# Optimization experiments

Hardware: AMD Instinct MI355X
Metric: run time of the kernel (lower is better)

Reference implementation:

```python
import jax, jax.numpy as jnp
import numpy as np

N, E, F_IN, HID, L, G, FFN = 100000, 1600000, 64, 128, 4, 512, 300
BN_EPS = 1e-5


def setup_inputs() -> dict:
    key = jax.random.key(0)
    ks = jax.random.split(key, 16)
    s = 0.05
    inp = {}
    inp["x"] = jax.random.normal(ks[0], (N, F_IN), dtype=jnp.float32)
    inp["edge_index"] = jax.random.randint(ks[1], (2, E), 0, N)
    inp["batch"] = jnp.sort(jax.random.randint(ks[2], (N,), 0, G))
    inp["enc_W"] = jax.random.normal(ks[3], (F_IN, HID), dtype=jnp.float32) * s
    inp["enc_b"] = jnp.zeros((HID,), jnp.float32)
    inp["Ws"] = jax.random.normal(ks[4], (L, HID, HID), dtype=jnp.float32) * s
    inp["bs"] = jnp.zeros((L, HID), jnp.float32)
    inp["bn_gamma"] = jnp.ones((L, HID), jnp.float32)
    inp["bn_beta"] = jnp.zeros((L, HID), jnp.float32)
    inp["bn_mean"] = jax.random.normal(ks[5], (L, HID), dtype=jnp.float32) * 0.01
    inp["bn_var"] = jnp.ones((L, HID), jnp.float32)
    inp["mlp_W0"] = jax.random.normal(ks[6], (HID, FFN), dtype=jnp.float32) * s
    inp["mlp_b0"] = jnp.zeros((FFN,), jnp.float32)
    inp["mlp_W1"] = jax.random.normal(ks[7], (FFN, FFN), dtype=jnp.float32) * s
    inp["mlp_b1"] = jnp.zeros((FFN,), jnp.float32)
    inp["mlp_W2"] = jax.random.normal(ks[8], (FFN, 1), dtype=jnp.float32) * s
    inp["mlp_b2"] = jnp.zeros((1,), jnp.float32)
    return inp


def reference(x, edge_index, batch, enc_W, enc_b, Ws, bs, bn_gamma, bn_beta,
              bn_mean, bn_var, mlp_W0, mlp_b0, mlp_W1, mlp_b1, mlp_W2, mlp_b2):
    # --- GCN normalization with self-loops (constant wrt params) ---
    loop = jnp.arange(N)
    row = jnp.concatenate([edge_index[0], loop])  # source
    col = jnp.concatenate([edge_index[1], loop])  # target (aggregation)
    deg = jax.ops.segment_sum(jnp.ones((E + N,), jnp.float32), col, num_segments=N)
    dinv = jnp.where(deg > 0, jax.lax.rsqrt(deg), 0.0)
    norm = dinv[row] * dinv[col]  # [E+N]

    # node encoder
    h = x @ enc_W + enc_b  # [N, HID]

    for i in range(L):
        h_prev = h
        # GCNConv: D^-1/2 (A+I) D^-1/2 (h W) + b
        hw = h @ Ws[i]
        msg = norm[:, None] * hw[row]                      # [E+N, HID]
        h = jax.ops.segment_sum(msg, col, num_segments=N) + bs[i]
        # BatchNorm1d (eval mode, running stats)
        h = (h - bn_mean[i]) * jax.lax.rsqrt(bn_var[i] + BN_EPS) * bn_gamma[i] + bn_beta[i]
        h = jax.nn.relu(h)
        if i > 0:
            h = h + h_prev

    # global mean pool over graphs
    sums = jax.ops.segment_sum(h, batch, num_segments=G)   # [G, HID]
    cnts = jax.ops.segment_sum(jnp.ones((N,), jnp.float32), batch, num_segments=G)
    gfeat = sums / jnp.maximum(cnts, 1.0)[:, None]

    # output MLP
    o = jax.nn.relu(gfeat @ mlp_W0 + mlp_b0)
    o = jax.nn.relu(o @ mlp_W1 + mlp_b1)
    return o @ mlp_W2 + mlp_b2  # [G, 1]
```

## Files before the change

### kernel.cpp

```cpp
#include <hip/hip_runtime.h>
#include <hip/hip_fp16.h>

#define NN 100000
#define NE 1600000
#define FIN 64
#define HID 128
#define NL 4
#define NG 512
#define FFN 300
#define BN_EPS 1e-5f
#define LDH 136
#define NB 512
#define NPB 196
#define CURPAD 16

static inline size_t alignup(size_t x) { return (x + 255) & ~(size_t)255; }

struct half8 { __half2 h[4]; };

typedef _Float16 f16;
typedef __attribute__((ext_vector_type(8))) _Float16 f16x8;
typedef __attribute__((ext_vector_type(4))) float f32x4;

__global__ __launch_bounds__(1024) void k_bcount(const int* __restrict__ col,
                                                 int* __restrict__ bcnt) {
    __shared__ int h[NB];
    int t = threadIdx.x;
    if (t < NB) h[t] = 0;
    __syncthreads();
    for (int e = blockIdx.x * 1024 + t; e < NE; e += 256 * 1024)
        atomicAdd(&h[col[e] / NPB], 1);
    __syncthreads();
    if (t < NB && h[t] > 0) atomicAdd(&bcnt[t], h[t]);
}

__global__ void k_bscan(const int* __restrict__ bcnt, int* __restrict__ bbase,
                        int* __restrict__ bcur) {
    __shared__ int s[NB];
    int t = threadIdx.x;
    int v = bcnt[t];
    s[t] = v;
    __syncthreads();
    for (int off = 1; off < NB; off <<= 1) {
        int u = (t >= off) ? s[t - off] : 0;
        __syncthreads();
        s[t] += u;
        __syncthreads();
    }
    int excl = s[t] - v;
    bbase[t] = excl;
    bcur[t * CURPAD] = excl;
    if (t == NB - 1) bbase[NB] = s[t];
}

__global__ void k_bscatter(const int* __restrict__ row, const int* __restrict__ col,
                           int* __restrict__ bcur, int* __restrict__ ebuf) {
    int e = blockIdx.x * 256 + threadIdx.x;
    if (e >= NE) return;
    int c = col[e];
    int b = c / NPB;
    int pos = atomicAdd(&bcur[b * CURPAD], 1);
    ebuf[pos] = row[e] | ((c - b * NPB) << 17);
}

__global__ __launch_bounds__(256) void k_binfill(const int* __restrict__ ebuf,
                                                 const int* __restrict__ bbase,
                                                 int* __restrict__ offs,
                                                 int* __restrict__ ends,
                                                 float* __restrict__ dinv,
                                                 int* __restrict__ csr_src) {
    __shared__ int cnt[NPB];
    __shared__ int scn[256];
    __shared__ int cur[NPB];
    int b = blockIdx.x, t = threadIdx.x;
    int lo = b * NPB;
    int hi = lo + NPB; if (hi > NN) hi = NN;
    int n = hi - lo;
    if (n <= 0) return;
    int s0 = bbase[b], s1 = bbase[b + 1];
    for (int i = t; i < NPB; i += 256) cnt[i] = 0;
    __syncthreads();
    for (int j = s0 + t; j < s1; j += 256)
        atomicAdd(&cnt[((unsigned)ebuf[j]) >> 17], 1);
    __syncthreads();
    int v = (t < n) ? cnt[t] : 0;
    scn[t] = v;
    __syncthreads();
    for (int off = 1; off < 256; off <<= 1) {
        int u = (t >= off) ? scn[t - off] : 0;
        __syncthreads();
        scn[t] += u;
        __syncthreads();
    }
    if (t < n) {
        int g = s0 + scn[t] - v;
        offs[lo + t] = g;
        ends[lo + t] = g + v;
        dinv[lo + t] = rsqrtf((float)(v + 1));
        cur[t] = g;
    }
    __syncthreads();
    for (int j = s0 + t; j < s1; j += 256) {
        int e = ebuf[j];
        int pos = atomicAdd(&cur[((unsigned)e) >> 17], 1);
        csr_src[pos] = e & 0x1FFFF;
    }
}

__global__ __launch_bounds__(256) void k_enc(const float* __restrict__ x,
                                             const float* __restrict__ W,
                                             const float* __restrict__ b,
                                             __half* __restrict__ h) {
    __shared__ float sW[FIN * HID];
    __shared__ float sx[64 * (FIN + 1)];
    int t = threadIdx.x;
    int row0 = blockIdx.x * 64;
    for (int i = t; i < FIN * HID; i += 256) sW[i] = W[i];
    for (int i = t; i < 64 * FIN; i += 256) {
        int r = i >> 6, k = i & 63;
        sx[r * (FIN + 1) + k] = (row0 + r < NN) ? x[(size_t)(row0 + r) * FIN + k] : 0.0f;
    }
    __syncthreads();
    int tx = t & 15, ty = t >> 4;
    int j0 = tx * 8, r0 = ty * 4;
    float acc[4][8];
    #pragma unroll
    for (int r = 0; r < 4; ++r)
        #pragma unroll
        for (int j = 0; j < 8; ++j) acc[r][j] = 0.0f;
    for (int k = 0; k < FIN; ++k) {
        float xv[4];
        #pragma unroll
        for (int r = 0; r < 4; ++r) xv[r] = sx[(r0 + r) * (FIN + 1) + k];
        float4 w0 = *(const float4*)&sW[k * HID + j0];
        float4 w1 = *(const float4*)&sW[k * HID + j0 + 4];
        float wv[8] = {w0.x, w0.y, w0.z, w0.w, w1.x, w1.y, w1.z, w1.w};
        #pragma unroll
        for (int r = 0; r < 4; ++r)
            #pragma unroll
            for (int j = 0; j < 8; ++j) acc[r][j] += xv[r] * wv[j];
    }
    #pragma unroll
    for (int r = 0; r < 4; ++r) {
        int rowi = row0 + r0 + r;
        if (rowi < NN) {
            half8 o;
            #pragma unroll
            for (int p = 0; p < 4; ++p)
                o.h[p] = __floats2half2_rn(acc[r][2 * p] + b[j0 + 2 * p],
                                           acc[r][2 * p + 1] + b[j0 + 2 * p + 1]);
            *(half8*)&h[(size_t)rowi * HID + j0] = o;
        }
    }
}

__global__ void k_convW(const float* __restrict__ Ws, f16* __restrict__ wt) {
    int tid = blockIdx.x * 256 + threadIdx.x;
    for (int i = tid; i < NL * HID * HID; i += 64 * 256) {
        int l = i >> 14, rem = i & 16383;
        int c = rem >> 7, k = rem & 127;
        wt[i] = (f16)Ws[(l << 14) + k * HID + c];
    }
}

__global__ __launch_bounds__(256) void k_gemm_mfma(const __half* __restrict__ h,
                                                   const f16* __restrict__ wt,
                                                   const float* __restrict__ dinv,
                                                   __half* __restrict__ hw) {
    __shared__ f16 sh[64 * LDH];
    __shared__ f16 sw[128 * LDH];
    int t = threadIdx.x;
    int row0 = blockIdx.x * 64;
    for (int idx = t; idx < 64 * 16; idx += 256) {
        int r = idx >> 4, ch = (idx & 15) * 8;
        f16x8 v = {0, 0, 0, 0, 0, 0, 0, 0};
        if (row0 + r < NN) v = *(const f16x8*)(h + (size_t)(row0 + r) * HID + ch);
        *(f16x8*)&sh[r * LDH + ch] = v;
    }
    for (int idx = t; idx < 128 * 16; idx += 256) {
        int c = idx >> 4, ch = (idx & 15) * 8;
        *(f16x8*)&sw[c * LDH + ch] = *(const f16x8*)(wt + c * HID + ch);
    }
    __syncthreads();
    int w = t >> 6, lane = t & 63;
    int lrow = lane & 15, lk = (lane >> 4) * 8;
    f32x4 acc[8];
    #pragma unroll
    for (int ct = 0; ct < 8; ++ct) acc[ct] = (f32x4){0.0f, 0.0f, 0.0f, 0.0f};
    const f16* pa = &sh[(w * 16 + lrow) * LDH + lk];
    #pragma unroll
    for (int ks = 0; ks < 4; ++ks) {
        f16x8 a = *(const f16x8*)(pa + ks * 32);
        #pragma unroll
        for (int ct = 0; ct < 8; ++ct) {
            f16x8 b = *(const f16x8*)&sw[(ct * 16 + lrow) * LDH + ks * 32 + lk];
            acc[ct] = __builtin_amdgcn_mfma_f32_16x16x32_f16(a, b, acc[ct], 0, 0, 0);
        }
    }
    int rbase = row0 + w * 16 + (lane >> 4) * 4;
    #pragma unroll
    for (int i = 0; i < 4; ++i) {
        int grow = rbase + i;
        if (grow < NN) {
            float dv = dinv[grow];
            #pragma unroll
            for (int ct = 0; ct < 8; ++ct)
                hw[(size_t)grow * HID + ct * 16 + lrow] = __float2half(dv * acc[ct][i]);
        }
    }
}

__device__ __forceinline__ void add8(float* a, float4 raw) {
    const __half2* p = (const __half2*)&raw;
    #pragma unroll
    for (int q = 0; q < 4; ++q) {
        float2 u = __half22float2(p[q]);
        a[2 * q] += u.x;
        a[2 * q + 1] += u.y;
    }
}

__global__ __launch_bounds__(256) void k_gather(
    const int* __restrict__ offs, const int* __restrict__ ends,
    const int* __restrict__ csr_src,
    const float* __restrict__ dinv,
    const __half* __restrict__ hw, const __half* __restrict__ hprev,
    const float* __restrict__ bias, const float* __restrict__ gamma,
    const float* __restrict__ beta, const float* __restrict__ mean,
    const float* __restrict__ var,
    __half* __restrict__ hout, int with_res) {
    int node = (blockIdx.x * 256 + threadIdx.x) >> 6;
    if (node >= NN) return;
    int lane = threadIdx.x & 63;
    int grp = lane >> 4;
    int fb = (lane & 15) * 8;
    int s = offs[node], e = ends[node];
    float a[8] = {0, 0, 0, 0, 0, 0, 0, 0};
    int j = s + grp;
    for (; j + 4 < e; j += 8) {
        int s0 = csr_src[j], s1 = csr_src[j + 4];
        float4 r0 = *(const float4*)(hw + (size_t)s0 * HID + fb);
        float4 r1 = *(const float4*)(hw + (size_t)s1 * HID + fb);
        add8(a, r0);
        add8(a, r1);
    }
    for (; j < e; j += 4) {
        int s0 = csr_src[j];
        float4 r0 = *(const float4*)(hw + (size_t)s0 * HID + fb);
        add8(a, r0);
    }
    #pragma unroll
    for (int q = 0; q < 8; ++q) {
        a[q] += __shfl_xor(a[q], 16);
        a[q] += __shfl_xor(a[q], 32);
    }
    if (grp) return;
    float4 sraw = *(const float4*)(hw + (size_t)node * HID + fb);
    add8(a, sraw);
    float dc = dinv[node];
    float4 bi0 = *(const float4*)(bias + fb),  bi1 = *(const float4*)(bias + fb + 4);
    float4 mn0 = *(const float4*)(mean + fb),  mn1 = *(const float4*)(mean + fb + 4);
    float4 vr0 = *(const float4*)(var + fb),   vr1 = *(const float4*)(var + fb + 4);
    float4 gm0 = *(const float4*)(gamma + fb), gm1 = *(const float4*)(gamma + fb + 4);
    float4 bt0 = *(const float4*)(beta + fb),  bt1 = *(const float4*)(beta + fb + 4);
    float bi[8] = {bi0.x, bi0.y, bi0.z, bi0.w, bi1.x, bi1.y, bi1.z, bi1.w};
    float mn[8] = {mn0.x, mn0.y, mn0.z, mn0.w, mn1.x, mn1.y, mn1.z, mn1.w};
    float vr[8] = {vr0.x, vr0.y, vr0.z, vr0.w, vr1.x, vr1.y, vr1.z, vr1.w};
    float gm[8] = {gm0.x, gm0.y, gm0.z, gm0.w, gm1.x, gm1.y, gm1.z, gm1.w};
    float bt[8] = {bt0.x, bt0.y, bt0.z, bt0.w, bt1.x, bt1.y, bt1.z, bt1.w};
    float o[8];
    #pragma unroll
    for (int q = 0; q < 8; ++q)
        o[q] = fmaxf((dc * a[q] + bi[q] - mn[q]) * rsqrtf(vr[q] + BN_EPS) * gm[q] + bt[q], 0.0f);
    if (with_res) {
        float4 praw = *(const float4*)(hprev + (size_t)node * HID + fb);
        const __half2* pp = (const __half2*)&praw;
        #pragma unroll
        for (int q = 0; q < 4; ++q) {
            float2 p = __half22float2(pp[q]);
            o[2 * q] += p.x;
            o[2 * q + 1] += p.y;
        }
    }
    half8 ov;
    #pragma unroll
    for (int q = 0; q < 4; ++q)
        ov.h[q] = __floats2half2_rn(o[2 * q], o[2 * q + 1]);
    *(half8*)(hout + (size_t)node * HID + fb) = ov;
}

__device__ __forceinline__ int lower_bound_dev(const int* __restrict__ a, int n, int v) {
    int lo = 0, hi = n;
    while (lo < hi) {
        int m = (lo + hi) >> 1;
        if (a[m] < v) lo = m + 1; else hi = m;
    }
    return lo;
}

__global__ __launch_bounds__(256) void k_pool_seg(const __half* __restrict__ h,
                                                  const int* __restrict__ batch,
                                                  float* __restrict__ gfeat) {
    __shared__ int range[2];
    __shared__ float s[256];
    int g = blockIdx.x, t = threadIdx.x;
    if (t == 0) {
        range[0] = lower_bound_dev(batch, NN, g);
        range[1] = lower_bound_dev(batch, NN, g + 1);
    }
    __syncthreads();
    int start = range[0], end = range[1];
    int f = t & 127, half = t >> 7;
    float acc = 0.0f;
    for (int i = start + half; i < end; i += 2)
        acc += __half2float(h[(size_t)i * HID + f]);
    s[t] = acc;
    __syncthreads();
    if (t < 128) {
        float sum = s[t] + s[t + 128];
        float cnt = (float)(end - start);
        gfeat[(size_t)g * HID + t] = sum / fmaxf(cnt, 1.0f);
    }
}

__global__ void k_mlp0(const float* __restrict__ gfeat,
                       const float* __restrict__ W, const float* __restrict__ b,
                       float* __restrict__ out) {
    __shared__ float srow[HID];
    int g = blockIdx.x, t = threadIdx.x;
    if (t < HID) srow[t] = gfeat[(size_t)g * HID + t];
    __syncthreads();
    for (int j = t; j < FFN; j += 128) {
        float acc = b[j];
        for (int k = 0; k < HID; ++k) acc += srow[k] * W[k * FFN + j];
        out[(size_t)g * FFN + j] = fmaxf(acc, 0.0f);
    }
}

__global__ void k_mlp1(const float* __restrict__ in, const float* __restrict__ W,
                       const float* __restrict__ b, float* __restrict__ out) {
    __shared__ float srow[FFN];
    int g = blockIdx.x, t = threadIdx.x;
    for (int k = t; k < FFN; k += 128) srow[k] = in[(size_t)g * FFN + k];
    __syncthreads();
    for (int j = t; j < FFN; j += 128) {
        float acc = b[j];
        for (int k = 0; k < FFN; ++k) acc += srow[k] * W[k * FFN + j];
        out[(size_t)g * FFN + j] = fmaxf(acc, 0.0f);
    }
}

__global__ void k_mlp2(const float* __restrict__ in, const float* __restrict__ W,
                       const float* __restrict__ b, float* __restrict__ out) {
    int g = blockIdx.x, lane = threadIdx.x;
    float acc = 0.0f;
    for (int k = lane; k < FFN; k += 64) acc += in[(size_t)g * FFN + k] * W[k];
    for (int off = 32; off > 0; off >>= 1) acc += __shfl_down(acc, off);
    if (lane == 0) out[g] = acc + b[0];
}

extern "C" void kernel_launch(void* const* d_in, const int* in_sizes, int n_in,
                              void* d_out, int out_size, void* d_ws, size_t ws_size,
                              hipStream_t stream) {
    const float* x    = (const float*)d_in[0];
    const int*   ei   = (const int*)d_in[1];
    const int*   batch= (const int*)d_in[2];
    const float* encW = (const float*)d_in[3];
    const float* encb = (const float*)d_in[4];
    const float* Ws   = (const float*)d_in[5];
    const float* bs   = (const float*)d_in[6];
    const float* gam  = (const float*)d_in[7];
    const float* bet  = (const float*)d_in[8];
    const float* mean = (const float*)d_in[9];
    const float* var  = (const float*)d_in[10];
    const float* W0   = (const float*)d_in[11];
    const float* b0   = (const float*)d_in[12];
    const float* W1   = (const float*)d_in[13];
    const float* b1   = (const float*)d_in[14];
    const float* W2   = (const float*)d_in[15];
    const float* b2   = (const float*)d_in[16];
    float* out = (float*)d_out;

    char* w = (char*)d_ws;
    float*  dinv    = (float*)w;  w += alignup((size_t)NN * 4);
    int*    offs    = (int*)w;    w += alignup((size_t)NN * 4);
    int*    ends    = (int*)w;    w += alignup((size_t)NN * 4);
    int*    csr_src = (int*)w;    w += alignup((size_t)NE * 4);
    int*    bcnt    = (int*)w;    w += alignup((size_t)NB * 4);
    int*    bbase   = (int*)w;    w += alignup((size_t)(NB + 1) * 4);
    int*    bcur    = (int*)w;    w += alignup((size_t)NB * CURPAD * 4);
    int*    ebuf    = (int*)w;    w += alignup((size_t)NE * 4);
    __half* hA      = (__half*)w; w += alignup((size_t)NN * HID * 2);
    __half* hB      = (__half*)w; w += alignup((size_t)NN * HID * 2);
    __half* hw_     = (__half*)w; w += alignup((size_t)NN * HID * 2);
    f16*    wt      = (f16*)w;    w += alignup((size_t)NL * HID * HID * 2);
    float*  gfeat   = (float*)w;  w += alignup((size_t)NG * HID * 4);
    float*  m0      = (float*)w;  w += alignup((size_t)NG * FFN * 4);
    float*  m1      = (float*)w;  w += alignup((size_t)NG * FFN * 4);

    const int* row = ei;
    const int* col = ei + NE;

    hipMemsetAsync(bcnt, 0, (size_t)NB * 4, stream);
    k_bcount<<<256, 1024, 0, stream>>>(col, bcnt);
    k_bscan<<<1, NB, 0, stream>>>(bcnt, bbase, bcur);
    k_bscatter<<<(NE + 255) / 256, 256, 0, stream>>>(row, col, bcur, ebuf);
    k_binfill<<<NB, 256, 0, stream>>>(ebuf, bbase, offs, ends, dinv, csr_src);

    k_convW<<<64, 256, 0, stream>>>(Ws, wt);
    k_enc<<<(NN + 63) / 64, 256, 0, stream>>>(x, encW, encb, hA);

    __half* hcur = hA;
    __half* hnext = hB;
    for (int l = 0; l < NL; ++l) {
        k_gemm_mfma<<<(NN + 63) / 64, 256, 0, stream>>>(hcur, wt + (size_t)l * HID * HID, dinv, hw_);
        k_gather<<<(NN * 64 + 255) / 256, 256, 0, stream>>>(
            offs, ends, csr_src, dinv, hw_, hcur,
            bs + l * HID, gam + l * HID, bet + l * HID, mean + l * HID, var + l * HID,
            hnext, l > 0 ? 1 : 0);
        __half* tmp = hcur; hcur = hnext; hnext = tmp;
    }

    k_pool_seg<<<NG, 256, 0, stream>>>(hcur, batch, gfeat);
    k_mlp0<<<NG, 128, 0, stream>>>(gfeat, W0, b0, m0);
    k_mlp1<<<NG, 128, 0, stream>>>(m0, W1, b1, m1);
    k_mlp2<<<NG, 64, 0, stream>>>(m1, W2, b2, out);
}
```

Baseline: 595.0 us.

## Use MFMA encoder, block-aggregated edge scatter, and deeper gather unrolling

Replaces the FP32 scalar encoder GEMM with an FP16 MFMA kernel that uses a pre-transposed FP16 encoder weight prepared in k_convW. Changes the bucket scatter so each block first builds a shared-memory histogram and then does one global atomic per bucket, instead of one global atomic per edge. Adds a 4-way unrolled gather loop so more neighbour loads are in flight at once. Running the encoder in FP16 costs some precision, and the encoder now writes scalar half stores that are not coalesced.

```diff
diff --git a/kernel.cpp b/kernel.cpp
--- a/kernel.cpp
+++ b/kernel.cpp
@@ -19,6 +19,7 @@
 struct half8 { __half2 h[4]; };
 
 typedef _Float16 f16;
+typedef __attribute__((ext_vector_type(4))) _Float16 f16x4;
 typedef __attribute__((ext_vector_type(8))) _Float16 f16x8;
 typedef __attribute__((ext_vector_type(4))) float f32x4;
 
@@ -53,14 +54,39 @@
     if (t == NB - 1) bbase[NB] = s[t];
 }
 
-__global__ void k_bscatter(const int* __restrict__ row, const int* __restrict__ col,
-                           int* __restrict__ bcur, int* __restrict__ ebuf) {
-    int e = blockIdx.x * 256 + threadIdx.x;
-    if (e >= NE) return;
-    int c = col[e];
-    int b = c / NPB;
-    int pos = atomicAdd(&bcur[b * CURPAD], 1);
-    ebuf[pos] = row[e] | ((c - b * NPB) << 17);
+__global__ __launch_bounds__(1024) void k_bscatter2(const int* __restrict__ row,
+                                                    const int* __restrict__ col,
+                                                    int* __restrict__ bcur,
+                                                    int* __restrict__ ebuf) {
+    __shared__ int hcnt[NB];
+    __shared__ int hbase[NB];
+    int t = threadIdx.x;
+    int e0 = blockIdx.x * 4096;
+    if (t < NB) hcnt[t] = 0;
+    __syncthreads();
+    #pragma unroll
+    for (int k = 0; k < 4; ++k) {
+        int e = e0 + k * 1024 + t;
+        if (e < NE) atomicAdd(&hcnt[col[e] / NPB], 1);
+    }
+    __syncthreads();
+    if (t < NB) {
+        int c = hcnt[t];
+        hbase[t] = (c > 0) ? atomicAdd(&bcur[t * CURPAD], c) : 0;
+    }
+    __syncthreads();
+    if (t < NB) hcnt[t] = 0;
+    __syncthreads();
+    #pragma unroll
+    for (int k = 0; k < 4; ++k) {
+        int e = e0 + k * 1024 + t;
+        if (e < NE) {
+            int c = col[e];
+            int b = c / NPB;
+            int loc = atomicAdd(&hcnt[b], 1);
+            ebuf[hbase[b] + loc] = row[e] | ((c - b * NPB) << 17);
+        }
+    }
 }
 
 __global__ __launch_bounds__(256) void k_binfill(const int* __restrict__ ebuf,
@@ -107,59 +133,67 @@
     }
 }
 
-__global__ __launch_bounds__(256) void k_enc(const float* __restrict__ x,
-                                             const float* __restrict__ W,
-                                             const float* __restrict__ b,
-                                             __half* __restrict__ h) {
-    __shared__ float sW[FIN * HID];
-    __shared__ float sx[64 * (FIN + 1)];
-    int t = threadIdx.x;
-    int row0 = blockIdx.x * 64;
-    for (int i = t; i < FIN * HID; i += 256) sW[i] = W[i];
-    for (int i = t; i < 64 * FIN; i += 256) {
-        int r = i >> 6, k = i & 63;
-        sx[r * (FIN + 1) + k] = (row0 + r < NN) ? x[(size_t)(row0 + r) * FIN + k] : 0.0f;
-    }
-    __syncthreads();
-    int tx = t & 15, ty = t >> 4;
-    int j0 = tx * 8, r0 = ty * 4;
-    float acc[4][8];
-    #pragma unroll
-    for (int r = 0; r < 4; ++r)
-        #pragma unroll
-        for (int j = 0; j < 8; ++j) acc[r][j] = 0.0f;
-    for (int k = 0; k < FIN; ++k) {
-        float xv[4];
-        #pragma unroll
-        for (int r = 0; r < 4; ++r) xv[r] = sx[(r0 + r) * (FIN + 1) + k];
-        float4 w0 = *(const float4*)&sW[k * HID + j0];
-        float4 w1 = *(const float4*)&sW[k * HID + j0 + 4];
-        float wv[8] = {w0.x, w0.y, w0.z, w0.w, w1.x, w1.y, w1.z, w1.w};
-        #pragma unroll
-        for (int r = 0; r < 4; ++r)
-            #pragma unroll
-            for (int j = 0; j < 8; ++j) acc[r][j] += xv[r] * wv[j];
-    }
-    #pragma unroll
-    for (int r = 0; r < 4; ++r) {
-        int rowi = row0 + r0 + r;
-        if (rowi < NN) {
-            half8 o;
-            #pragma unroll
-            for (int p = 0; p < 4; ++p)
-                o.h[p] = __floats2half2_rn(acc[r][2 * p] + b[j0 + 2 * p],
-                                           acc[r][2 * p + 1] + b[j0 + 2 * p + 1]);
-            *(half8*)&h[(size_t)rowi * HID + j0] = o;
-        }
-    }
-}
-
-__global__ void k_convW(const float* __restrict__ Ws, f16* __restrict__ wt) {
+__global__ void k_convW(const float* __restrict__ Ws, const float* __restrict__ encW,
+                        f16* __restrict__ wt, f16* __restrict__ wte) {
     int tid = blockIdx.x * 256 + threadIdx.x;
     for (int i = tid; i < NL * HID * HID; i += 64 * 256) {
         int l = i >> 14, rem = i & 16383;
         int c = rem >> 7, k = rem & 127;
         wt[i] = (f16)Ws[(l << 14) + k * HID + c];
+    }
+    for (int i = tid; i < HID * FIN; i += 64 * 256) {
+        int c = i >> 6, k = i & 63;
+        wte[i] = (f16)encW[k * HID + c];
+    }
+}
+
+__global__ __launch_bounds__(256) void k_enc_mfma(const float* __restrict__ x,
+                                                  const f16* __restrict__ wte,
+                                                  const float* __restrict__ b,
+                                                  __half* __restrict__ h) {
+    __shared__ f16 sx[64 * 72];
+    __shared__ f16 sw[128 * 72];
+    int t = threadIdx.x;
+    int row0 = blockIdx.x * 64;
+    for (int idx = t; idx < 64 * 16; idx += 256) {
+        int r = idx >> 4, c4 = (idx & 15) * 4;
+        float4 v = {0.0f, 0.0f, 0.0f, 0.0f};
+        if (row0 + r < NN) v = *(const float4*)(x + (size_t)(row0 + r) * FIN + c4);
+        f16x4 o = {(f16)v.x, (f16)v.y, (f16)v.z, (f16)v.w};
+        *(f16x4*)&sx[r * 72 + c4] = o;
+    }
+    for (int idx = t; idx < 128 * 8; idx += 256) {
+        int c = idx >> 3, ch = (idx & 7) * 8;
+        *(f16x8*)&sw[c * 72 + ch] = *(const f16x8*)(wte + c * FIN + ch);
+    }
+    __syncthreads();
+    int w = t >> 6, lane = t & 63;
+    int lrow = lane & 15, lk = (lane >> 4) * 8;
+    f32x4 acc[8];
+    #pragma unroll
+    for (int ct = 0; ct < 8; ++ct) acc[ct] = (f32x4){0.0f, 0.0f, 0.0f, 0.0f};
+    const f16* pa = &sx[(w * 16 + lrow) * 72 + lk];
+    #pragma unroll
+    for (int ks = 0; ks < 2; ++ks) {
+        f16x8 a = *(const f16x8*)(pa + ks * 32);
+        #pragma unroll
+        for (int ct = 0; ct < 8; ++ct) {
+            f16x8 bb = *(const f16x8*)&sw[(ct * 16 + lrow) * 72 + ks * 32 + lk];
+            acc[ct] = __builtin_amdgcn_mfma_f32_16x16x32_f16(a, bb, acc[ct], 0, 0, 0);
+        }
+    }
+    float bv[8];
+    #pragma unroll
+    for (int ct = 0; ct < 8; ++ct) bv[ct] = b[ct * 16 + lrow];
+    int rbase = row0 + w * 16 + (lane >> 4) * 4;
+    #pragma unroll
+    for (int i = 0; i < 4; ++i) {
+        int grow = rbase + i;
+        if (grow < NN) {
+            #pragma unroll
+            for (int ct = 0; ct < 8; ++ct)
+                h[(size_t)grow * HID + ct * 16 + lrow] = __float2half(acc[ct][i] + bv[ct]);
+        }
     }
 }
 
@@ -237,12 +271,19 @@
     int s = offs[node], e = ends[node];
     float a[8] = {0, 0, 0, 0, 0, 0, 0, 0};
     int j = s + grp;
+    for (; j + 12 < e; j += 16) {
+        int s0 = csr_src[j], s1 = csr_src[j + 4], s2 = csr_src[j + 8], s3 = csr_src[j + 12];
+        float4 r0 = *(const float4*)(hw + (size_t)s0 * HID + fb);
+        float4 r1 = *(const float4*)(hw + (size_t)s1 * HID + fb);
+        float4 r2 = *(const float4*)(hw + (size_t)s2 * HID + fb);
+        float4 r3 = *(const float4*)(hw + (size_t)s3 * HID + fb);
+        add8(a, r0); add8(a, r1); add8(a, r2); add8(a, r3);
+    }
     for (; j + 4 < e; j += 8) {
         int s0 = csr_src[j], s1 = csr_src[j + 4];
         float4 r0 = *(const float4*)(hw + (size_t)s0 * HID + fb);
         float4 r1 = *(const float4*)(hw + (size_t)s1 * HID + fb);
-        add8(a, r0);
-        add8(a, r1);
+        add8(a, r0); add8(a, r1);
     }
     for (; j < e; j += 4) {
         int s0 = csr_src[j];
@@ -394,6 +435,7 @@
     __half* hB      = (__half*)w; w += alignup((size_t)NN * HID * 2);
     __half* hw_     = (__half*)w; w += alignup((size_t)NN * HID * 2);
     f16*    wt      = (f16*)w;    w += alignup((size_t)NL * HID * HID * 2);
+    f16*    wte     = (f16*)w;    w += alignup((size_t)HID * FIN * 2);
     float*  gfeat   = (float*)w;  w += alignup((size_t)NG * HID * 4);
     float*  m0      = (float*)w;  w += alignup((size_t)NG * FFN * 4);
     float*  m1      = (float*)w;  w += alignup((size_t)NG * FFN * 4);
@@ -404,11 +446,11 @@
     hipMemsetAsync(bcnt, 0, (size_t)NB * 4, stream);
     k_bcount<<<256, 1024, 0, stream>>>(col, bcnt);
     k_bscan<<<1, NB, 0, stream>>>(bcnt, bbase, bcur);
-    k_bscatter<<<(NE + 255) / 256, 256, 0, stream>>>(row, col, bcur, ebuf);
+    k_bscatter2<<<(NE + 4095) / 4096, 1024, 0, stream>>>(row, col, bcur, ebuf);
     k_binfill<<<NB, 256, 0, stream>>>(ebuf, bbase, offs, ends, dinv, csr_src);
 
-    k_convW<<<64, 256, 0, stream>>>(Ws, wt);
-    k_enc<<<(NN + 63) / 64, 256, 0, stream>>>(x, encW, encb, hA);
+    k_convW<<<64, 256, 0, stream>>>(Ws, encW, wt, wte);
+    k_enc_mfma<<<(NN + 63) / 64, 256, 0, stream>>>(x, wte, encb, hA);
 
     __half* hcur = hA;
     __half* hnext = hB;
```

Result: faster. 523.9 us (median of 2 runs) (-12.0%).
